# Optimization experiments

Hardware: AMD Instinct MI355X
Metric: run time of the kernel (lower is better)

## Reference

```python
import jax, jax.numpy as jnp
import numpy as np


def _layernorm(x, g, b, eps=1e-5):
    mu = jnp.mean(x, axis=-1, keepdims=True)
    xc = x - mu
    var = jnp.mean(xc * xc, axis=-1, keepdims=True)
    return xc * jax.lax.rsqrt(var + eps) * g + b


def _s5(u, Lambda_re, Lambda_im, B_re, B_im, C_re, C_im, Dskip, log_step):
    # Diagonal complex SSM with ZOH discretization (S5).
    Lam = Lambda_re + 1j * Lambda_im                       # (P,) complex64
    Lam_bar = jnp.exp(Lam * jnp.exp(log_step))             # (P,)
    B_bar = ((Lam_bar - 1.0) / Lam)[:, None] * (B_re + 1j * B_im)  # (P, D)
    Bu = jnp.einsum('bld,pd->blp', u.astype(jnp.complex64), B_bar)  # (B, L, P)
    A = jnp.broadcast_to(Lam_bar, Bu.shape)

    def combine(e1, e2):
        a1, b1 = e1
        a2, b2 = e2
        return a1 * a2, a2 * b1 + b2

    _, xs = jax.lax.associative_scan(combine, (A, Bu), axis=1)  # parallel scan over L
    y = 2.0 * jnp.real(jnp.einsum('blp,dp->bld', xs, C_re + 1j * C_im))
    return y + Dskip * u


def setup_inputs() -> dict:
    key = jax.random.key(0)
    ks = jax.random.split(key, 10)
    B, L, D, P = 4, 2048, 1024, 64
    F = int(D * 2.0)  # ff_mult = 2.0
    x = jax.random.normal(ks[0], (B, L, D), jnp.float32)
    ln1_g = jnp.ones((D,), jnp.float32)
    ln1_b = jnp.zeros((D,), jnp.float32)
    ln2_g = jnp.ones((D,), jnp.float32)
    ln2_b = jnp.zeros((D,), jnp.float32)
    Lambda_re = -(0.5 + jax.random.uniform(ks[1], (P,), jnp.float32))  # stable poles
    Lambda_im = jnp.pi * jnp.arange(P, dtype=jnp.float32)              # HiPPO-like spread
    B_re = jax.random.normal(ks[2], (P, D), jnp.float32) / np.float32(np.sqrt(D))
    B_im = jax.random.normal(ks[3], (P, D), jnp.float32) / np.float32(np.sqrt(D))
    C_re = jax.random.normal(ks[4], (D, P), jnp.float32) / np.float32(np.sqrt(P))
    C_im = jax.random.normal(ks[5], (D, P), jnp.float32) / np.float32(np.sqrt(P))
    Dskip = jax.random.normal(ks[6], (D,), jnp.float32)
    dt_min, dt_max = 1e-3, 1e-1
    log_step = (np.float32(np.log(dt_min))
                + jax.random.uniform(ks[7], (P,), jnp.float32)
                * np.float32(np.log(dt_max) - np.log(dt_min)))
    W_enc = jax.random.normal(ks[8], (2 * F, D), jnp.float32) / np.float32(np.sqrt(D))
    W_dec = jax.random.normal(ks[9], (D, F), jnp.float32) / np.float32(np.sqrt(F))
    return dict(x=x, ln1_g=ln1_g, ln1_b=ln1_b, ln2_g=ln2_g, ln2_b=ln2_b,
                Lambda_re=Lambda_re, Lambda_im=Lambda_im, B_re=B_re, B_im=B_im,
                C_re=C_re, C_im=C_im, Dskip=Dskip, log_step=log_step,
                W_enc=W_enc, W_dec=W_dec)


def reference(x, ln1_g, ln1_b, ln2_g, ln2_b, Lambda_re, Lambda_im, B_re, B_im,
              C_re, C_im, Dskip, log_step, W_enc, W_dec):
    # S5Block: pre-LN -> S5 -> GELU -> residual (dropout = identity in eval)
    fx = _layernorm(x, ln1_g, ln1_b)
    h = jax.nn.gelu(_s5(fx, Lambda_re, Lambda_im, B_re, B_im, C_re, C_im, Dskip, log_step),
                    approximate=False) + fx
    # pre-LN GEGLU feed-forward -> residual
    fx2 = _layernorm(h, ln2_g, ln2_b)
    e = fx2 @ W_enc.T                      # (B, L, 2F)
    a, gate = jnp.split(e, 2, axis=-1)
    e = a * jax.nn.gelu(gate, approximate=False)
    return e @ W_dec.T + fx2
```

## Files before the change

kernel.cpp:

```cpp
#include <hip/hip_runtime.h>
#include <hip/hip_bf16.h>
#include <math.h>

typedef unsigned short u16;
typedef __bf16 v8bf __attribute__((ext_vector_type(8)));
typedef float f32x4 __attribute__((ext_vector_type(4)));

__device__ __forceinline__ float us2f(u16 h) {
    union { unsigned int u; float f; } v; v.u = ((unsigned int)h) << 16; return v.f;
}
__device__ __forceinline__ u16 f2us(float f) {
    union { float f; unsigned int u; } v; v.f = f;
    unsigned int r = v.u + 0x7fffu + ((v.u >> 16) & 1u);
    return (u16)(r >> 16);
}
__device__ __forceinline__ float gelu_f(float x) {
    return 0.5f * x * (1.0f + erff(x * 0.70710678118654752f));
}
__device__ __forceinline__ void gload_lds16(const u16* g, u16* l) {
    auto gp = reinterpret_cast<const __attribute__((address_space(1))) unsigned int*>(
        (uintptr_t)g);
    auto lp = reinterpret_cast<__attribute__((address_space(3))) unsigned int*>(
        (uintptr_t)l);
    __builtin_amdgcn_global_load_lds(gp, lp, 16, 0, 0);
}

__global__ __launch_bounds__(256) void prepall_kernel(
    const float* __restrict__ Wenc, u16* __restrict__ WeB,
    const float* __restrict__ Wdec, u16* __restrict__ WdB,
    const float* __restrict__ Lre, const float* __restrict__ Lim,
    const float* __restrict__ lstep,
    const float* __restrict__ Bre, const float* __restrict__ Bim,
    const float* __restrict__ Cre, const float* __restrict__ Cim,
    u16* __restrict__ Bbar, u16* __restrict__ C2)
{
    const int b = blockIdx.x, tid = threadIdx.x;
    if (b < 3072) {
        const float* in = (b < 2048) ? Wenc : Wdec;
        u16* outp = (b < 2048) ? WeB : WdB;
        const int i = (b < 2048 ? b : b - 2048) * 2048 + tid * 8;
        float4 a = *reinterpret_cast<const float4*>(in + i);
        float4 c = *reinterpret_cast<const float4*>(in + i + 4);
        u16 o[8] = { f2us(a.x), f2us(a.y), f2us(a.z), f2us(a.w),
                     f2us(c.x), f2us(c.y), f2us(c.z), f2us(c.w) };
        *reinterpret_cast<uint4*>(outp + i) = *reinterpret_cast<uint4*>(o);
        return;
    }
    const int idx = (b - 3072) * 256 + tid;
    if (idx < 65536) {
        const int p = idx >> 10, d = idx & 1023;
        const float lr = Lre[p], li = Lim[p];
        const float dt = expf(lstep[p]);
        const float er = expf(lr * dt);
        const float ar = er * cosf(li * dt), ai = er * sinf(li * dt);
        const float nr = ar - 1.0f, ni = ai;
        const float den = lr * lr + li * li;
        const float cr = (nr * lr + ni * li) / den;
        const float ci = (ni * lr - nr * li) / den;
        const float br = Bre[idx], bi = Bim[idx];
        Bbar[p * 1024 + d]        = f2us(cr * br - ci * bi);
        Bbar[(64 + p) * 1024 + d] = f2us(cr * bi + ci * br);
    } else {
        const int i = idx - 65536;
        const int d = i >> 6, p = i & 63;
        C2[d * 128 + p]      = f2us( 2.0f * Cre[i]);
        C2[d * 128 + 64 + p] = f2us(-2.0f * Cim[i]);
    }
}

template<typename TIN>
__global__ __launch_bounds__(256) void ln_kernel(const TIN* __restrict__ in,
                                                 const float* __restrict__ g,
                                                 const float* __restrict__ b,
                                                 u16* __restrict__ out)
{
    const int row = blockIdx.x, tid = threadIdx.x;
    const size_t base = (size_t)row * 1024 + tid * 4;
    float x0, x1, x2, x3;
    if constexpr (sizeof(TIN) == 4) {
        float4 v = *reinterpret_cast<const float4*>(in + base);
        x0 = v.x; x1 = v.y; x2 = v.z; x3 = v.w;
    } else {
        ushort4 v = *reinterpret_cast<const ushort4*>((const u16*)in + base);
        x0 = us2f(v.x); x1 = us2f(v.y); x2 = us2f(v.z); x3 = us2f(v.w);
    }
    float s = x0 + x1 + x2 + x3;
    float q = x0*x0 + x1*x1 + x2*x2 + x3*x3;
    #pragma unroll
    for (int o = 32; o; o >>= 1) { s += __shfl_down(s, o); q += __shfl_down(q, o); }
    __shared__ float red[8];
    if ((tid & 63) == 0) { red[tid >> 6] = s; red[4 + (tid >> 6)] = q; }
    __syncthreads();
    s = red[0] + red[1] + red[2] + red[3];
    q = red[4] + red[5] + red[6] + red[7];
    const float mu = s * (1.0f / 1024.0f);
    const float rs = rsqrtf(q * (1.0f / 1024.0f) - mu * mu + 1e-5f);
    float4 gv = *reinterpret_cast<const float4*>(g + tid * 4);
    float4 bv = *reinterpret_cast<const float4*>(b + tid * 4);
    ushort4 o4;
    o4.x = f2us((x0 - mu) * rs * gv.x + bv.x);
    o4.y = f2us((x1 - mu) * rs * gv.y + bv.y);
    o4.z = f2us((x2 - mu) * rs * gv.z + bv.z);
    o4.w = f2us((x3 - mu) * rs * gv.w + bv.w);
    *reinterpret_cast<ushort4*>(out + base) = o4;
}

__global__ __launch_bounds__(256) void scan_kernel(
    const float* __restrict__ Bu,
    const float* __restrict__ Lre, const float* __restrict__ Lim,
    const float* __restrict__ lstep,
    u16* __restrict__ A2)
{
    const int b = blockIdx.x >> 6;
    const int p = blockIdx.x & 63;
    const int t = threadIdx.x;
    const float lr = Lre[p], li = Lim[p];
    const float dt = expf(lstep[p]);
    const float er = expf(lr * dt);
    const float ar = er * cosf(li * dt), ai = er * sinf(li * dt);

    const size_t base = ((size_t)b * 2048 + t * 8) * 128;
    float xr[8], xi[8];
    float sr = 0.f, si = 0.f;
    #pragma unroll
    for (int i = 0; i < 8; ++i) {
        const float br = Bu[base + i * 128 + p];
        const float bi = Bu[base + i * 128 + 64 + p];
        const float nr = ar * sr - ai * si + br;
        const float ni = ar * si + ai * sr + bi;
        sr = nr; si = ni;
        xr[i] = sr; xi[i] = si;
    }
    float fr = ar, fi = ai;
    #pragma unroll
    for (int s = 0; s < 3; ++s) { const float t2 = fr*fr - fi*fi; fi = 2.f*fr*fi; fr = t2; }
    __shared__ float Er[256], Ei[256];
    Er[t] = sr; Ei[t] = si;
    __syncthreads();
    float vr = sr, vi = si;
    for (int off = 1; off < 256; off <<= 1) {
        float pr = 0.f, pi = 0.f;
        if (t >= off) { pr = Er[t - off]; pi = Ei[t - off]; }
        __syncthreads();
        vr += fr * pr - fi * pi;
        vi += fr * pi + fi * pr;
        Er[t] = vr; Ei[t] = vi;
        const float nf = fr*fr - fi*fi; fi = 2.f*fr*fi; fr = nf;
        __syncthreads();
    }
    float cr = 0.f, ci = 0.f;
    if (t > 0) { cr = Er[t - 1]; ci = Ei[t - 1]; }
    float gr = ar * cr - ai * ci, gi = ar * ci + ai * cr;
    #pragma unroll
    for (int i = 0; i < 8; ++i) {
        xr[i] += gr; xi[i] += gi;
        const float n2 = ar * gr - ai * gi; gi = ar * gi + ai * gr; gr = n2;
    }
    #pragma unroll
    for (int i = 0; i < 8; ++i) {
        const size_t m = (size_t)b * 2048 + t * 8 + i;
        A2[m * 128 + p]      = f2us(xr[i]);
        A2[m * 128 + 64 + p] = f2us(xi[i]);
    }
}

template<int BM, int BN>
__global__ __launch_bounds__(64) void gemm_small_kernel(
    const u16* __restrict__ A, const u16* __restrict__ B, float* __restrict__ Cout,
    const int N, const int K)
{
    __shared__ u16 lsA[BM * 32];
    __shared__ u16 lsB[BN * 32];
    const int tid = threadIdx.x;
    const int lane = tid & 63;
    const int m0 = blockIdx.y * BM, n0 = blockIdx.x * BN;
    f32x4 acc[4][4] = {};
    for (int k0 = 0; k0 < K; k0 += 32) {
        #pragma unroll
        for (int j = 0; j < 4; ++j) {
            const int s = j * 64 + tid;
            gload_lds16(A + (size_t)(m0 + (s >> 2)) * K + k0 + (s & 3) * 8,
                        lsA + (s - lane) * 8);
            gload_lds16(B + (size_t)(n0 + (s >> 2)) * K + k0 + (s & 3) * 8,
                        lsB + (s - lane) * 8);
        }
        __syncthreads();
        v8bf af[4], bfv[4];
        #pragma unroll
        for (int f = 0; f < 4; ++f)
            af[f] = *reinterpret_cast<const v8bf*>(
                lsA + (f * 16 + (lane & 15)) * 32 + (lane >> 4) * 8);
        #pragma unroll
        for (int f = 0; f < 4; ++f)
            bfv[f] = *reinterpret_cast<const v8bf*>(
                lsB + (f * 16 + (lane & 15)) * 32 + (lane >> 4) * 8);
        #pragma unroll
        for (int fm = 0; fm < 4; ++fm)
            #pragma unroll
            for (int fn = 0; fn < 4; ++fn)
                acc[fm][fn] = __builtin_amdgcn_mfma_f32_16x16x32_bf16(
                    af[fm], bfv[fn], acc[fm][fn], 0, 0, 0);
        __syncthreads();
    }
    #pragma unroll
    for (int fm = 0; fm < 4; ++fm)
    #pragma unroll
    for (int fn = 0; fn < 4; ++fn)
    #pragma unroll
    for (int i = 0; i < 4; ++i) {
        const int r = m0 + fm * 16 + (lane >> 4) * 4 + i;
        const int c = n0 + fn * 16 + (lane & 15);
        Cout[(size_t)r * N + c] = acc[fm][fn][i];
    }
}

#define BAR_MMA_BEGIN \
    __builtin_amdgcn_s_barrier(); \
    asm volatile("s_waitcnt lgkmcnt(0)" ::: "memory"); \
    __builtin_amdgcn_sched_barrier(0); \
    __builtin_amdgcn_s_setprio(1);
#define MMA_END  __builtin_amdgcn_s_setprio(0);
#define ENDBAR   __builtin_amdgcn_s_barrier();
#define VMK(n)   asm volatile("s_waitcnt vmcnt(" #n ")" ::: "memory");

#define STAGE(s, bi) do { \
    u16* d0_ = lds + (bi) * BUFE + ((s) * 128 + (wid * 2 + 0) * 8) * 64; \
    u16* d1_ = lds + (bi) * BUFE + ((s) * 128 + (wid * 2 + 1) * 8) * 64; \
    gload_lds16(pS[s][0], d0_); gload_lds16(pS[s][1], d1_); \
    pS[s][0] += 64; pS[s][1] += 64; } while (0)

template<int MFB>
__device__ __forceinline__ void glu_read_a(const u16* cb, int wm, int l15, int lg,
                                           int l7, v8bf (&af)[2][2])
{
    #pragma unroll
    for (int j = 0; j < 2; ++j) {
        const int row = wm * 128 + (MFB + j) * 16 + l15;
        #pragma unroll
        for (int kk = 0; kk < 2; ++kk)
            af[j][kk] = *reinterpret_cast<const v8bf*>(
                cb + row * 64 + (((kk * 4 + lg) ^ l7) * 8));
    }
}
__device__ __forceinline__ void glu_read_b(const u16* cb, int wn, int l15, int lg,
                                           int l7, v8bf (&bf)[2][2][2])
{
    #pragma unroll
    for (int cf = 0; cf < 2; ++cf)
    #pragma unroll
    for (int ag = 0; ag < 2; ++ag)
    #pragma unroll
    for (int kk = 0; kk < 2; ++kk) {
        const int rb = ag * 128 + wn * 32 + cf * 16 + l15;
        bf[cf][ag][kk] = *reinterpret_cast<const v8bf*>(
            cb + (256 + rb) * 64 + (((kk * 4 + lg) ^ l7) * 8));
    }
}
template<int MFB>
__device__ __forceinline__ void glu_mma(const v8bf (&af)[2][2], const v8bf (&bf)[2][2][2],
                                        f32x4 (&accA)[8][2], f32x4 (&accG)[8][2])
{
    #pragma unroll
    for (int j = 0; j < 2; ++j)
    #pragma unroll
    for (int cf = 0; cf < 2; ++cf)
    #pragma unroll
    for (int kk = 0; kk < 2; ++kk) {
        accA[MFB + j][cf] = __builtin_amdgcn_mfma_f32_16x16x32_bf16(
            af[j][kk], bf[cf][0][kk], accA[MFB + j][cf], 0, 0, 0);
        accG[MFB + j][cf] = __builtin_amdgcn_mfma_f32_16x16x32_bf16(
            af[j][kk], bf[cf][1][kk], accG[MFB + j][cf], 0, 0, 0);
    }
}

template<int NBX>
__global__ __launch_bounds__(512, 2) void geglu8p_kernel(
    const u16* __restrict__ A, const u16* __restrict__ Bm, u16* __restrict__ Cout,
    const int K, const int NO, const int NT)
{
    constexpr int BUFE = 512 * 64;
    __shared__ u16 lds[2 * BUFE];
    const int tid = threadIdx.x, lane = tid & 63, wid = tid >> 6;
    const int wm = wid >> 2, wn = wid & 3;
    const int l15 = lane & 15, lg = lane >> 4, l7 = lane & 7;
    const int bid = blockIdx.x;
    const int swz = (bid & 7) * (NBX * 4) + (bid >> 3);
    const int by = swz / NBX, bx = swz % NBX;
    const int m0 = by * 256, n0 = bx * 128;

    const int rl = lane >> 3;
    const int scol = ((lane & 7) ^ rl) * 8;
    const u16* pS[4][2];
    #pragma unroll
    for (int j = 0; j < 2; ++j) {
        const int rloc = (wid * 2 + j) * 8 + rl;
        pS[0][j] = A  + (size_t)(m0 + rloc)       * K + scol;
        pS[1][j] = A  + (size_t)(m0 + 128 + rloc) * K + scol;
        pS[2][j] = Bm + (size_t)(n0 + rloc)       * K + scol;
        pS[3][j] = Bm + (size_t)(NO + n0 + rloc)  * K + scol;
    }

    f32x4 accA[8][2] = {};
    f32x4 accG[8][2] = {};

    #pragma unroll
    for (int t = 0; t < 2; ++t) {
        STAGE(0, t); STAGE(1, t); STAGE(2, t); STAGE(3, t);
    }
    VMK(0);
    __builtin_amdgcn_s_barrier();

    const int NI = NT >> 1;
    for (int i = 0; i < NI; ++i) {
        const bool s1 = (i > 0);
        const bool s2 = (2 * i + 2 < NT);
        const bool s3 = (2 * i + 3 < NT);
        {
            const u16* cb = lds;
            v8bf bf[2][2][2];
            v8bf af[2][2];
            glu_read_a<0>(cb, wm, l15, lg, l7, af);
            glu_read_b(cb, wn, l15, lg, l7, bf);
            if (s1) STAGE(0, 1);
            BAR_MMA_BEGIN; glu_mma<0>(af, bf, accA, accG); MMA_END; ENDBAR;
            glu_read_a<2>(cb, wm, l15, lg, l7, af);
            if (s1) STAGE(1, 1);
            BAR_MMA_BEGIN; glu_mma<2>(af, bf, accA, accG); MMA_END; ENDBAR;
            glu_read_a<4>(cb, wm, l15, lg, l7, af);
            if (s2) STAGE(2, 0);
            BAR_MMA_BEGIN; glu_mma<4>(af, bf, accA, accG); MMA_END; ENDBAR;
            glu_read_a<6>(cb, wm, l15, lg, l7, af);
            if (s2) STAGE(3, 0);
            BAR_MMA_BEGIN; glu_mma<6>(af, bf, accA, accG); MMA_END;
            if (s2) { VMK(4); } else { VMK(0); }
            ENDBAR;
        }
        {
            const u16* cb = lds + BUFE;
            v8bf bf[2][2][2];
            v8bf af[2][2];
            glu_read_a<0>(cb, wm, l15, lg, l7, af);
            glu_read_b(cb, wn, l15, lg, l7, bf);
            if (s2) STAGE(0, 0);
            BAR_MMA_BEGIN; glu_mma<0>(af, bf, accA, accG); MMA_END; ENDBAR;
            glu_read_a<2>(cb, wm, l15, lg, l7, af);
            if (s2) STAGE(1, 0);
            BAR_MMA_BEGIN; glu_mma<2>(af, bf, accA, accG); MMA_END; ENDBAR;
            glu_read_a<4>(cb, wm, l15, lg, l7, af);
            if (s3) STAGE(2, 1);
            BAR_MMA_BEGIN; glu_mma<4>(af, bf, accA, accG); MMA_END; ENDBAR;
            glu_read_a<6>(cb, wm, l15, lg, l7, af);
            if (s3) STAGE(3, 1);
            BAR_MMA_BEGIN; glu_mma<6>(af, bf, accA, accG); MMA_END;
            if (s3) { VMK(4); } else { VMK(0); }
            ENDBAR;
        }
    }

    #pragma unroll
    for (int mf = 0; mf < 8; ++mf)
    #pragma unroll
    for (int cf = 0; cf < 2; ++cf)
    #pragma unroll
    for (int q = 0; q < 4; ++q) {
        const int r = m0 + wm * 128 + mf * 16 + lg * 4 + q;
        const int c = n0 + wn * 32 + cf * 16 + l15;
        Cout[(size_t)r * NO + c] = f2us(accA[mf][cf][q] * gelu_f(accG[mf][cf][q]));
    }
}

template<int MFB, bool READB>
__device__ __forceinline__ void p4_read(const u16* cb, int wm, int wn, int l15,
                                        int lg, int l7, v8bf (&af)[4][2], v8bf (&bf)[2][2])
{
    #pragma unroll
    for (int j = 0; j < 4; ++j) {
        const int row = wm * 128 + (MFB + j) * 16 + l15;
        #pragma unroll
        for (int kk = 0; kk < 2; ++kk)
            af[j][kk] = *reinterpret_cast<const v8bf*>(
                cb + row * 64 + (((kk * 4 + lg) ^ l7) * 8));
    }
    if constexpr (READB) {
        #pragma unroll
        for (int cf = 0; cf < 2; ++cf)
        #pragma unroll
        for (int kk = 0; kk < 2; ++kk) {
            const int rb = wn * 32 + cf * 16 + l15;
            bf[cf][kk] = *reinterpret_cast<const v8bf*>(
                cb + (256 + rb) * 64 + (((kk * 4 + lg) ^ l7) * 8));
        }
    }
}
template<int MFB>
__device__ __forceinline__ void p4_mma(const v8bf (&af)[4][2], const v8bf (&bf)[2][2],
                                       f32x4 (&accA)[8][2])
{
    #pragma unroll
    for (int j = 0; j < 4; ++j)
    #pragma unroll
    for (int cf = 0; cf < 2; ++cf)
    #pragma unroll
    for (int kk = 0; kk < 2; ++kk)
        accA[MFB + j][cf] = __builtin_amdgcn_mfma_f32_16x16x32_bf16(
            af[j][kk], bf[cf][kk], accA[MFB + j][cf], 0, 0, 0);
}

template<int EPI, int NBX>
__global__ __launch_bounds__(512, 2) void gemm4p_kernel(
    const u16* __restrict__ A, const u16* __restrict__ Bm, void* __restrict__ Cout,
    const int K, const int NO, const int NT,
    const u16* __restrict__ aux, const float* __restrict__ dskip)
{
    constexpr int BUFE = 384 * 64;
    __shared__ u16 lds[2 * BUFE];
    const int tid = threadIdx.x, lane = tid & 63, wid = tid >> 6;
    const int wm = wid >> 2, wn = wid & 3;
    const int l15 = lane & 15, lg = lane >> 4, l7 = lane & 7;
    const int bid = blockIdx.x;
    const int swz = (bid & 7) * (NBX * 4) + (bid >> 3);
    const int by = swz / NBX, bx = swz % NBX;
    const int m0 = by * 256, n0 = bx * 128;

    const int rl = lane >> 3;
    const int scol = ((lane & 7) ^ rl) * 8;
    const u16* pS[3][2];
    #pragma unroll
    for (int j = 0; j < 2; ++j) {
        const int rloc = (wid * 2 + j) * 8 + rl;
        pS[0][j] = A  + (size_t)(m0 + rloc)       * K + scol;
        pS[1][j] = A  + (size_t)(m0 + 128 + rloc) * K + scol;
        pS[2][j] = Bm + (size_t)(n0 + rloc)       * K + scol;
    }

    f32x4 accA[8][2] = {};

    #pragma unroll
    for (int t = 0; t < 2; ++t) { STAGE(0, t); STAGE(1, t); STAGE(2, t); }
    VMK(0);
    __builtin_amdgcn_s_barrier();

    const int NI = NT >> 1;
    for (int i = 0; i < NI; ++i) {
        const bool s1 = (i > 0);
        const bool s2 = (2 * i + 2 < NT);
        const bool s3 = (2 * i + 3 < NT);
        v8bf af[4][2], bf[2][2];
        p4_read<0, true>(lds, wm, wn, l15, lg, l7, af, bf);
        if (s1) { STAGE(0, 1); STAGE(1, 1); }
        BAR_MMA_BEGIN; p4_mma<0>(af, bf, accA); MMA_END; ENDBAR;
        p4_read<4, false>(lds, wm, wn, l15, lg, l7, af, bf);
        if (s2) STAGE(2, 0);
        BAR_MMA_BEGIN; p4_mma<4>(af, bf, accA); MMA_END;
        if (s2) { VMK(2); } else { VMK(0); }
        ENDBAR;
        p4_read<0, true>(lds + BUFE, wm, wn, l15, lg, l7, af, bf);
        if (s2) { STAGE(0, 0); STAGE(1, 0); }
        BAR_MMA_BEGIN; p4_mma<0>(af, bf, accA); MMA_END; ENDBAR;
        p4_read<4, false>(lds + BUFE, wm, wn, l15, lg, l7, af, bf);
        if (s3) STAGE(2, 1);
        BAR_MMA_BEGIN; p4_mma<4>(af, bf, accA); MMA_END;
        if (s3) { VMK(2); } else { VMK(0); }
        ENDBAR;
    }

    #pragma unroll
    for (int mf = 0; mf < 8; ++mf)
    #pragma unroll
    for (int cf = 0; cf < 2; ++cf)
    #pragma unroll
    for (int q = 0; q < 4; ++q) {
        const int r = m0 + wm * 128 + mf * 16 + lg * 4 + q;
        const int c = n0 + wn * 32 + cf * 16 + l15;
        const size_t o = (size_t)r * NO + c;
        const float v = accA[mf][cf][q];
        if constexpr (EPI == 1) {
            const float u = us2f(aux[o]);
            const float t2 = v + dskip[c] * u;
            ((u16*)Cout)[o] = f2us(gelu_f(t2) + u);
        } else {
            ((float*)Cout)[o] = v + us2f(aux[o]);
        }
    }
}

static constexpr size_t OFF_FX  = 0;
static constexpr size_t OFF_BU  = 16777216;
static constexpr size_t OFF_A2  = 20971520;
static constexpr size_t OFF_E2  = 0;
static constexpr size_t OFF_FX2 = 33554432;
static constexpr size_t OFF_BB  = 50331648;
static constexpr size_t OFF_C2  = 50593792;
static constexpr size_t OFF_WE  = 50855936;
static constexpr size_t OFF_WD  = 59244544;

extern "C" void kernel_launch(void* const* d_in, const int* in_sizes, int n_in,
                              void* d_out, int out_size, void* d_ws, size_t ws_size,
                              hipStream_t stream) {
    const float* x    = (const float*)d_in[0];
    const float* l1g  = (const float*)d_in[1];
    const float* l1b  = (const float*)d_in[2];
    const float* l2g  = (const float*)d_in[3];
    const float* l2b  = (const float*)d_in[4];
    const float* Lre  = (const float*)d_in[5];
    const float* Lim  = (const float*)d_in[6];
    const float* Bre  = (const float*)d_in[7];
    const float* Bim  = (const float*)d_in[8];
    const float* Cre  = (const float*)d_in[9];
    const float* Cim  = (const float*)d_in[10];
    const float* Dsk  = (const float*)d_in[11];
    const float* lst  = (const float*)d_in[12];
    const float* Wenc = (const float*)d_in[13];
    const float* Wdec = (const float*)d_in[14];
    float* out = (float*)d_out;

    char* ws = (char*)d_ws;
    u16*   fx   = (u16*)(ws + OFF_FX);
    float* Bu   = (float*)(ws + OFF_BU);
    u16*   A2   = (u16*)(ws + OFF_A2);
    u16*   e2   = (u16*)(ws + OFF_E2);
    u16*   fx2  = (u16*)(ws + OFF_FX2);
    u16*   Bbar = (u16*)(ws + OFF_BB);
    u16*   C2   = (u16*)(ws + OFF_C2);
    u16*   WeB  = (u16*)(ws + OFF_WE);
    u16*   WdB  = (u16*)(ws + OFF_WD);
    u16*   h    = (u16*)d_out;

    ln_kernel<float><<<8192, 256, 0, stream>>>(x, l1g, l1b, fx);
    prepall_kernel<<<3584, 256, 0, stream>>>(Wenc, WeB, Wdec, WdB,
                                             Lre, Lim, lst, Bre, Bim, Cre, Cim,
                                             Bbar, C2);
    gemm_small_kernel<64, 64><<<dim3(2, 128), 64, 0, stream>>>(
        fx, Bbar, Bu, 128, 1024);
    scan_kernel<<<256, 256, 0, stream>>>(Bu, Lre, Lim, lst, A2);
    gemm4p_kernel<1, 8><<<256, 512, 0, stream>>>(
        A2, C2, h, 128, 1024, 2, fx, Dsk);
    ln_kernel<u16><<<8192, 256, 0, stream>>>(h, l2g, l2b, fx2);
    geglu8p_kernel<16><<<512, 512, 0, stream>>>(fx2, WeB, e2, 1024, 2048, 16);
    gemm4p_kernel<3, 8><<<256, 512, 0, stream>>>(
        e2, WdB, out, 2048, 1024, 32, fx2, nullptr);

    (void)in_sizes; (void)n_in; (void)out_size; (void)ws_size;
}
```

Before: 219.2 us.

## Switch GEGLU and projection GEMMs to 32x32x16 MFMA with restructured barrier schedule

```diff
diff --git a/kernel.cpp b/kernel.cpp
--- a/kernel.cpp
+++ b/kernel.cpp
@@ -5,6 +5,7 @@
 typedef unsigned short u16;
 typedef __bf16 v8bf __attribute__((ext_vector_type(8)));
 typedef float f32x4 __attribute__((ext_vector_type(4)));
+typedef float f32x16 __attribute__((ext_vector_type(16)));
 
 __device__ __forceinline__ float us2f(u16 h) {
     union { unsigned int u; float f; } v; v.u = ((unsigned int)h) << 16; return v.f;
@@ -214,64 +215,56 @@
     }
 }
 
-#define BAR_MMA_BEGIN \
-    __builtin_amdgcn_s_barrier(); \
-    asm volatile("s_waitcnt lgkmcnt(0)" ::: "memory"); \
-    __builtin_amdgcn_sched_barrier(0); \
-    __builtin_amdgcn_s_setprio(1);
-#define MMA_END  __builtin_amdgcn_s_setprio(0);
-#define ENDBAR   __builtin_amdgcn_s_barrier();
-#define VMK(n)   asm volatile("s_waitcnt vmcnt(" #n ")" ::: "memory");
-
+#define BARM()   asm volatile("s_barrier" ::: "memory")
+#define LGKM0()  asm volatile("s_waitcnt lgkmcnt(0)" ::: "memory")
+#define VMK(n)   asm volatile("s_waitcnt vmcnt(" #n ")" ::: "memory")
+#define PRIO1    __builtin_amdgcn_s_setprio(1)
+#define PRIO0    __builtin_amdgcn_s_setprio(0)
+#define MMA32(acc, a, b) \
+    acc = __builtin_amdgcn_mfma_f32_32x32x16_bf16(a, b, acc, 0, 0, 0)
+#define RDA(mf, kk) (*reinterpret_cast<const v8bf*>( \
+    cb + ((wm) * 128 + (mf) * 32 + l31) * 64 + ((((kk) * 2 + lh) ^ l7) * 8)))
+#define RDBG(ag, kk) (*reinterpret_cast<const v8bf*>( \
+    cb + (256 + (ag) * 128 + (wn) * 32 + l31) * 64 + ((((kk) * 2 + lh) ^ l7) * 8)))
+#define RDB4(kk) (*reinterpret_cast<const v8bf*>( \
+    cb + (256 + (wn) * 32 + l31) * 64 + ((((kk) * 2 + lh) ^ l7) * 8)))
 #define STAGE(s, bi) do { \
     u16* d0_ = lds + (bi) * BUFE + ((s) * 128 + (wid * 2 + 0) * 8) * 64; \
     u16* d1_ = lds + (bi) * BUFE + ((s) * 128 + (wid * 2 + 1) * 8) * 64; \
     gload_lds16(pS[s][0], d0_); gload_lds16(pS[s][1], d1_); \
     pS[s][0] += 64; pS[s][1] += 64; } while (0)
 
-template<int MFB>
-__device__ __forceinline__ void glu_read_a(const u16* cb, int wm, int l15, int lg,
-                                           int l7, v8bf (&af)[2][2])
-{
-    #pragma unroll
-    for (int j = 0; j < 2; ++j) {
-        const int row = wm * 128 + (MFB + j) * 16 + l15;
-        #pragma unroll
-        for (int kk = 0; kk < 2; ++kk)
-            af[j][kk] = *reinterpret_cast<const v8bf*>(
-                cb + row * 64 + (((kk * 4 + lg) ^ l7) * 8));
-    }
-}
-__device__ __forceinline__ void glu_read_b(const u16* cb, int wn, int l15, int lg,
-                                           int l7, v8bf (&bf)[2][2][2])
-{
-    #pragma unroll
-    for (int cf = 0; cf < 2; ++cf)
-    #pragma unroll
-    for (int ag = 0; ag < 2; ++ag)
-    #pragma unroll
-    for (int kk = 0; kk < 2; ++kk) {
-        const int rb = ag * 128 + wn * 32 + cf * 16 + l15;
-        bf[cf][ag][kk] = *reinterpret_cast<const v8bf*>(
-            cb + (256 + rb) * 64 + (((kk * 4 + lg) ^ l7) * 8));
-    }
-}
-template<int MFB>
-__device__ __forceinline__ void glu_mma(const v8bf (&af)[2][2], const v8bf (&bf)[2][2][2],
-                                        f32x4 (&accA)[8][2], f32x4 (&accG)[8][2])
-{
-    #pragma unroll
-    for (int j = 0; j < 2; ++j)
-    #pragma unroll
-    for (int cf = 0; cf < 2; ++cf)
-    #pragma unroll
-    for (int kk = 0; kk < 2; ++kk) {
-        accA[MFB + j][cf] = __builtin_amdgcn_mfma_f32_16x16x32_bf16(
-            af[j][kk], bf[cf][0][kk], accA[MFB + j][cf], 0, 0, 0);
-        accG[MFB + j][cf] = __builtin_amdgcn_mfma_f32_16x16x32_bf16(
-            af[j][kk], bf[cf][1][kk], accG[MFB + j][cf], 0, 0, 0);
-    }
-}
+#define GLU_HB(cb_, ab_, bb_, stA_, stB_) do { \
+    const u16* cb = (cb_); \
+    v8bf bfA[4], bfG[4], af[4]; \
+    _Pragma("unroll") for (int mf = 0; mf < 4; ++mf) af[mf] = RDA(mf, 0); \
+    _Pragma("unroll") for (int kk = 0; kk < 4; ++kk) { \
+        bfA[kk] = RDBG(0, kk); bfG[kk] = RDBG(1, kk); } \
+    if (stA_) STAGE(0, ab_); \
+    PRIO1; \
+    _Pragma("unroll") for (int mf = 0; mf < 4; ++mf) { \
+        MMA32(accA[mf], af[mf], bfA[0]); MMA32(accG[mf], af[mf], bfG[0]); } \
+    PRIO0; LGKM0(); BARM(); \
+    _Pragma("unroll") for (int mf = 0; mf < 4; ++mf) af[mf] = RDA(mf, 1); \
+    if (stA_) STAGE(1, ab_); \
+    PRIO1; \
+    _Pragma("unroll") for (int mf = 0; mf < 4; ++mf) { \
+        MMA32(accA[mf], af[mf], bfA[1]); MMA32(accG[mf], af[mf], bfG[1]); } \
+    PRIO0; LGKM0(); BARM(); \
+    _Pragma("unroll") for (int mf = 0; mf < 4; ++mf) af[mf] = RDA(mf, 2); \
+    if (stB_) STAGE(2, bb_); \
+    PRIO1; \
+    _Pragma("unroll") for (int mf = 0; mf < 4; ++mf) { \
+        MMA32(accA[mf], af[mf], bfA[2]); MMA32(accG[mf], af[mf], bfG[2]); } \
+    PRIO0; LGKM0(); BARM(); \
+    _Pragma("unroll") for (int mf = 0; mf < 4; ++mf) af[mf] = RDA(mf, 3); \
+    if (stB_) STAGE(3, bb_); \
+    PRIO1; \
+    _Pragma("unroll") for (int mf = 0; mf < 4; ++mf) { \
+        MMA32(accA[mf], af[mf], bfA[3]); MMA32(accG[mf], af[mf], bfG[3]); } \
+    PRIO0; LGKM0(); \
+    if (stB_) { VMK(4); } else { VMK(0); } \
+    BARM(); } while (0)
 
 template<int NBX>
 __global__ __launch_bounds__(512, 2) void geglu8p_kernel(
@@ -282,7 +275,7 @@
     __shared__ u16 lds[2 * BUFE];
     const int tid = threadIdx.x, lane = tid & 63, wid = tid >> 6;
     const int wm = wid >> 2, wn = wid & 3;
-    const int l15 = lane & 15, lg = lane >> 4, l7 = lane & 7;
+    const int l31 = lane & 31, lh = lane >> 5, l7 = lane & 7;
     const int bid = blockIdx.x;
     const int swz = (bid & 7) * (NBX * 4) + (bid >> 3);
     const int by = swz / NBX, bx = swz % NBX;
@@ -300,111 +293,53 @@
         pS[3][j] = Bm + (size_t)(NO + n0 + rloc)  * K + scol;
     }
 
-    f32x4 accA[8][2] = {};
-    f32x4 accG[8][2] = {};
-
-    #pragma unroll
-    for (int t = 0; t < 2; ++t) {
-        STAGE(0, t); STAGE(1, t); STAGE(2, t); STAGE(3, t);
-    }
+    f32x16 accA[4] = {};
+    f32x16 accG[4] = {};
+
+    #pragma unroll
+    for (int t = 0; t < 2; ++t) { STAGE(0, t); STAGE(1, t); STAGE(2, t); STAGE(3, t); }
     VMK(0);
-    __builtin_amdgcn_s_barrier();
+    BARM();
 
     const int NI = NT >> 1;
     for (int i = 0; i < NI; ++i) {
         const bool s1 = (i > 0);
         const bool s2 = (2 * i + 2 < NT);
         const bool s3 = (2 * i + 3 < NT);
-        {
-            const u16* cb = lds;
-            v8bf bf[2][2][2];
-            v8bf af[2][2];
-            glu_read_a<0>(cb, wm, l15, lg, l7, af);
-            glu_read_b(cb, wn, l15, lg, l7, bf);
-            if (s1) STAGE(0, 1);
-            BAR_MMA_BEGIN; glu_mma<0>(af, bf, accA, accG); MMA_END; ENDBAR;
-            glu_read_a<2>(cb, wm, l15, lg, l7, af);
-            if (s1) STAGE(1, 1);
-            BAR_MMA_BEGIN; glu_mma<2>(af, bf, accA, accG); MMA_END; ENDBAR;
-            glu_read_a<4>(cb, wm, l15, lg, l7, af);
-            if (s2) STAGE(2, 0);
-            BAR_MMA_BEGIN; glu_mma<4>(af, bf, accA, accG); MMA_END; ENDBAR;
-            glu_read_a<6>(cb, wm, l15, lg, l7, af);
-            if (s2) STAGE(3, 0);
-            BAR_MMA_BEGIN; glu_mma<6>(af, bf, accA, accG); MMA_END;
-            if (s2) { VMK(4); } else { VMK(0); }
-            ENDBAR;
-        }
-        {
-            const u16* cb = lds + BUFE;
-            v8bf bf[2][2][2];
-            v8bf af[2][2];
-            glu_read_a<0>(cb, wm, l15, lg, l7, af);
-            glu_read_b(cb, wn, l15, lg, l7, bf);
-            if (s2) STAGE(0, 0);
-            BAR_MMA_BEGIN; glu_mma<0>(af, bf, accA, accG); MMA_END; ENDBAR;
-            glu_read_a<2>(cb, wm, l15, lg, l7, af);
-            if (s2) STAGE(1, 0);
-            BAR_MMA_BEGIN; glu_mma<2>(af, bf, accA, accG); MMA_END; ENDBAR;
-            glu_read_a<4>(cb, wm, l15, lg, l7, af);
-            if (s3) STAGE(2, 1);
-            BAR_MMA_BEGIN; glu_mma<4>(af, bf, accA, accG); MMA_END; ENDBAR;
-            glu_read_a<6>(cb, wm, l15, lg, l7, af);
-            if (s3) STAGE(3, 1);
-            BAR_MMA_BEGIN; glu_mma<6>(af, bf, accA, accG); MMA_END;
-            if (s3) { VMK(4); } else { VMK(0); }
-            ENDBAR;
-        }
-    }
-
-    #pragma unroll
-    for (int mf = 0; mf < 8; ++mf)
-    #pragma unroll
-    for (int cf = 0; cf < 2; ++cf)
-    #pragma unroll
-    for (int q = 0; q < 4; ++q) {
-        const int r = m0 + wm * 128 + mf * 16 + lg * 4 + q;
-        const int c = n0 + wn * 32 + cf * 16 + l15;
-        Cout[(size_t)r * NO + c] = f2us(accA[mf][cf][q] * gelu_f(accG[mf][cf][q]));
-    }
-}
-
-template<int MFB, bool READB>
-__device__ __forceinline__ void p4_read(const u16* cb, int wm, int wn, int l15,
-                                        int lg, int l7, v8bf (&af)[4][2], v8bf (&bf)[2][2])
-{
-    #pragma unroll
-    for (int j = 0; j < 4; ++j) {
-        const int row = wm * 128 + (MFB + j) * 16 + l15;
-        #pragma unroll
-        for (int kk = 0; kk < 2; ++kk)
-            af[j][kk] = *reinterpret_cast<const v8bf*>(
-                cb + row * 64 + (((kk * 4 + lg) ^ l7) * 8));
-    }
-    if constexpr (READB) {
-        #pragma unroll
-        for (int cf = 0; cf < 2; ++cf)
-        #pragma unroll
-        for (int kk = 0; kk < 2; ++kk) {
-            const int rb = wn * 32 + cf * 16 + l15;
-            bf[cf][kk] = *reinterpret_cast<const v8bf*>(
-                cb + (256 + rb) * 64 + (((kk * 4 + lg) ^ l7) * 8));
-        }
-    }
-}
-template<int MFB>
-__device__ __forceinline__ void p4_mma(const v8bf (&af)[4][2], const v8bf (&bf)[2][2],
-                                       f32x4 (&accA)[8][2])
-{
-    #pragma unroll
-    for (int j = 0; j < 4; ++j)
-    #pragma unroll
-    for (int cf = 0; cf < 2; ++cf)
-    #pragma unroll
-    for (int kk = 0; kk < 2; ++kk)
-        accA[MFB + j][cf] = __builtin_amdgcn_mfma_f32_16x16x32_bf16(
-            af[j][kk], bf[cf][kk], accA[MFB + j][cf], 0, 0, 0);
-}
+        GLU_HB(lds,        1, 0, s1, s2);
+        GLU_HB(lds + BUFE, 0, 1, s2, s3);
+    }
+
+    #pragma unroll
+    for (int mf = 0; mf < 4; ++mf)
+    #pragma unroll
+    for (int q = 0; q < 16; ++q) {
+        const int r = m0 + wm * 128 + mf * 32 + (q & 3) + 8 * (q >> 2) + 4 * lh;
+        const int c = n0 + wn * 32 + l31;
+        Cout[(size_t)r * NO + c] = f2us(accA[mf][q] * gelu_f(accG[mf][q]));
+    }
+}
+
+#define P4_HB(cb_, ab_, bb_, stA_, stB_) do { \
+    const u16* cb = (cb_); \
+    v8bf bfv[4], af0[4], af1[4]; \
+    _Pragma("unroll") for (int mf = 0; mf < 4; ++mf) { \
+        af0[mf] = RDA(mf, 0); af1[mf] = RDA(mf, 1); } \
+    _Pragma("unroll") for (int kk = 0; kk < 4; ++kk) bfv[kk] = RDB4(kk); \
+    if (stA_) { STAGE(0, ab_); STAGE(1, ab_); } \
+    PRIO1; \
+    _Pragma("unroll") for (int mf = 0; mf < 4; ++mf) { \
+        MMA32(acc[mf], af0[mf], bfv[0]); MMA32(acc[mf], af1[mf], bfv[1]); } \
+    PRIO0; LGKM0(); BARM(); \
+    _Pragma("unroll") for (int mf = 0; mf < 4; ++mf) { \
+        af0[mf] = RDA(mf, 2); af1[mf] = RDA(mf, 3); } \
+    if (stB_) STAGE(2, bb_); \
+    PRIO1; \
+    _Pragma("unroll") for (int mf = 0; mf < 4; ++mf) { \
+        MMA32(acc[mf], af0[mf], bfv[2]); MMA32(acc[mf], af1[mf], bfv[3]); } \
+    PRIO0; LGKM0(); \
+    if (stB_) { VMK(2); } else { VMK(0); } \
+    BARM(); } while (0)
 
 template<int EPI, int NBX>
 __global__ __launch_bounds__(512, 2) void gemm4p_kernel(
@@ -416,7 +351,7 @@
     __shared__ u16 lds[2 * BUFE];
     const int tid = threadIdx.x, lane = tid & 63, wid = tid >> 6;
     const int wm = wid >> 2, wn = wid & 3;
-    const int l15 = lane & 15, lg = lane >> 4, l7 = lane & 7;
+    const int l31 = lane & 31, lh = lane >> 5, l7 = lane & 7;
     const int bid = blockIdx.x;
     const int swz = (bid & 7) * (NBX * 4) + (bid >> 3);
     const int by = swz / NBX, bx = swz % NBX;
@@ -433,47 +368,30 @@
         pS[2][j] = Bm + (size_t)(n0 + rloc)       * K + scol;
     }
 
-    f32x4 accA[8][2] = {};
+    f32x16 acc[4] = {};
 
     #pragma unroll
     for (int t = 0; t < 2; ++t) { STAGE(0, t); STAGE(1, t); STAGE(2, t); }
     VMK(0);
-    __builtin_amdgcn_s_barrier();
+    BARM();
 
     const int NI = NT >> 1;
     for (int i = 0; i < NI; ++i) {
         const bool s1 = (i > 0);
         const bool s2 = (2 * i + 2 < NT);
         const bool s3 = (2 * i + 3 < NT);
-        v8bf af[4][2], bf[2][2];
-        p4_read<0, true>(lds, wm, wn, l15, lg, l7, af, bf);
-        if (s1) { STAGE(0, 1); STAGE(1, 1); }
-        BAR_MMA_BEGIN; p4_mma<0>(af, bf, accA); MMA_END; ENDBAR;
-        p4_read<4, false>(lds, wm, wn, l15, lg, l7, af, bf);
-        if (s2) STAGE(2, 0);
-        BAR_MMA_BEGIN; p4_mma<4>(af, bf, accA); MMA_END;
-        if (s2) { VMK(2); } else { VMK(0); }
-        ENDBAR;
-        p4_read<0, true>(lds + BUFE, wm, wn, l15, lg, l7, af, bf);
-        if (s2) { STAGE(0, 0); STAGE(1, 0); }
-        BAR_MMA_BEGIN; p4_mma<0>(af, bf, accA); MMA_END; ENDBAR;
-        p4_read<4, false>(lds + BUFE, wm, wn, l15, lg, l7, af, bf);
-        if (s3) STAGE(2, 1);
-        BAR_MMA_BEGIN; p4_mma<4>(af, bf, accA); MMA_END;
-        if (s3) { VMK(2); } else { VMK(0); }
-        ENDBAR;
-    }
-
-    #pragma unroll
-    for (int mf = 0; mf < 8; ++mf)
-    #pragma unroll
-    for (int cf = 0; cf < 2; ++cf)
-    #pragma unroll
-    for (int q = 0; q < 4; ++q) {
-        const int r = m0 + wm * 128 + mf * 16 + lg * 4 + q;
-        const int c = n0 + wn * 32 + cf * 16 + l15;
+        P4_HB(lds,        1, 0, s1, s2);
+        P4_HB(lds + BUFE, 0, 1, s2, s3);
+    }
+
+    #pragma unroll
+    for (int mf = 0; mf < 4; ++mf)
+    #pragma unroll
+    for (int q = 0; q < 16; ++q) {
+        const int r = m0 + wm * 128 + mf * 32 + (q & 3) + 8 * (q >> 2) + 4 * lh;
+        const int c = n0 + wn * 32 + l31;
         const size_t o = (size_t)r * NO + c;
-        const float v = accA[mf][cf][q];
+        const float v = acc[mf][q];
         if constexpr (EPI == 1) {
             const float u = us2f(aux[o]);
             const float t2 = v + dskip[c] * u;
```

Result: slower. 230.4 us (+5.1%).
